# Performance work log

Hardware: AMD Instinct MI355X
Metric: run time of the kernel (lower is better)

## Reference

```python
import jax, jax.numpy as jnp
import numpy as np

N_NODES = 100000


def _gcn_conv(x, edge_index, W, b, n_nodes):
    """PyG GCNConv: add self-loops, symmetric deg^-1/2 normalization,
    linear transform, scatter-sum aggregation, bias."""
    loop = jnp.arange(n_nodes, dtype=edge_index.dtype)
    src = jnp.concatenate([edge_index[0], loop])  # message sources
    dst = jnp.concatenate([edge_index[1], loop])  # message targets
    deg = jax.ops.segment_sum(jnp.ones_like(dst, dtype=x.dtype), dst,
                              num_segments=n_nodes)
    dinv = jnp.where(deg > 0, jax.lax.rsqrt(jnp.maximum(deg, 1.0)), 0.0)
    norm = dinv[src] * dinv[dst]  # [E+N]
    h = x @ W  # [N, out] transform before aggregation (fewer bytes moved)
    msg = h[src] * norm[:, None]  # [E+N, out]
    out = jax.ops.segment_sum(msg, dst, num_segments=n_nodes)
    return out + b


def setup_inputs() -> dict:
    key = jax.random.key(0)
    k1, k2, k3, k4, k5, k6 = jax.random.split(key, 6)
    in_ch, hid, out_ch = 128, 64, 64
    x = jax.random.normal(k1, (N_NODES, in_ch), dtype=jnp.float32)
    edge_index = jax.random.randint(k2, (2, 3200000), 0, N_NODES, dtype=jnp.int64)
    # Glorot-style init for GCN weights, zeros for bias (PyG default)
    W1 = jax.random.normal(k3, (in_ch, hid), dtype=jnp.float32) / np.sqrt(in_ch)
    b1 = jnp.zeros((hid,), dtype=jnp.float32)
    W2 = jax.random.normal(k4, (hid, out_ch), dtype=jnp.float32) / np.sqrt(hid)
    b2 = jnp.zeros((out_ch,), dtype=jnp.float32)
    return {"x": x, "edge_index": edge_index, "W1": W1, "b1": b1,
            "W2": W2, "b2": b2}


def reference(x, edge_index, W1, b1, W2, b2):
    n = x.shape[0]
    h = _gcn_conv(x, edge_index, W1, b1, n)
    h = jax.nn.relu(h)
    out = _gcn_conv(h, edge_index, W2, b2, n)
    return out
```

## Files before the change

### kernel.cpp

```cpp
#include <hip/hip_runtime.h>
#include <math.h>


#define BKT_SHIFT 9
#define BKT_NODES 512
#define NBSH      256
#define CHUNK     8192
#define MAXB      20480

typedef unsigned short ushort_t;

static __device__ __forceinline__ unsigned short f2bf(float f) {
    unsigned u = __float_as_uint(f);
    unsigned r = (u + 0x7FFFu + ((u >> 16) & 1u)) >> 16;
    return (unsigned short)r;
}
static __device__ __forceinline__ float bf_lo(unsigned u) {
    return __uint_as_float(u << 16);
}
static __device__ __forceinline__ float bf_hi(unsigned u) {
    return __uint_as_float(u & 0xFFFF0000u);
}

struct ushort4_t { unsigned short x, y, z, w; };

__global__ __launch_bounds__(256) void zero_small(int* __restrict__ bhist,
                                                  int* __restrict__ bcur) {
    int t = threadIdx.x;
    bhist[t] = 0;
    bcur[t]  = 0;
}

__global__ __launch_bounds__(256) void coarse_hist(const int* __restrict__ dst,
                                                   int* __restrict__ bhist,
                                                   int E, int NB) {
    __shared__ int h[NBSH];
    const int t  = threadIdx.x;
    const int e0 = blockIdx.x * CHUNK;
    const int n  = min(CHUNK, E - e0);
    h[t] = 0;
    __syncthreads();
    for (int i = t; i < n; i += 256) atomicAdd(&h[dst[e0 + i] >> BKT_SHIFT], 1);
    __syncthreads();
    if (t < NB && h[t] > 0) atomicAdd(&bhist[t], h[t]);
}

__global__ __launch_bounds__(256) void scan196(const int* __restrict__ bhist,
                                               int* __restrict__ boffs, int NB, int E) {
    __shared__ int sh[256];
    int t = threadIdx.x;
    int orig = (t < NB) ? bhist[t] : 0;
    sh[t] = orig;
    __syncthreads();
    for (int d = 1; d < 256; d <<= 1) {
        int u = (t >= d) ? sh[t - d] : 0;
        __syncthreads();
        sh[t] += u;
        __syncthreads();
    }
    if (t < NB) boffs[t] = sh[t] - orig;
    if (t == NB) boffs[NB] = E;
    if (t == 255 && NB < 255) boffs[NB] = E;
}

__global__ __launch_bounds__(256) void bucket_bin(const int* __restrict__ src,
                                                  const int* __restrict__ dst,
                                                  const int* __restrict__ boffs,
                                                  int* __restrict__ bcur,
                                                  unsigned* __restrict__ pairs,
                                                  int E, int NB) {
    __shared__ unsigned stag[CHUNK];
    __shared__ int hist[NBSH];
    __shared__ int lofs[NBSH];
    __shared__ int lcur[NBSH];
    __shared__ int gbase[NBSH];
    const int t  = threadIdx.x;
    const int e0 = blockIdx.x * CHUNK;
    const int n  = min(CHUNK, E - e0);

    for (int i = t; i < NBSH; i += 256) hist[i] = 0;
    __syncthreads();
    for (int i = t; i < n; i += 256) atomicAdd(&hist[dst[e0 + i] >> BKT_SHIFT], 1);
    __syncthreads();
    int v = hist[t];
    lofs[t] = v;
    __syncthreads();
    for (int d = 1; d < 256; d <<= 1) {
        int u = (t >= d) ? lofs[t - d] : 0;
        __syncthreads();
        lofs[t] += u;
        __syncthreads();
    }
    if (t < NB) {
        lcur[t]  = lofs[t] - v;
        gbase[t] = (v > 0) ? boffs[t] + atomicAdd(&bcur[t], v) : 0;
    }
    __syncthreads();
    for (int i = t; i < n; i += 256) {
        int d = dst[e0 + i];
        int s = src[e0 + i];
        int b = d >> BKT_SHIFT;
        int p = atomicAdd(&lcur[b], 1);
        stag[p] = ((unsigned)(d & (BKT_NODES - 1)) << 17) | (unsigned)s;
    }
    __syncthreads();
    const int wv = t >> 6, ln = t & 63;
    for (int b = wv; b < NB; b += 4) {
        int cb = hist[b];
        if (cb == 0) continue;
        int lo = lofs[b] - cb;
        int gb = gbase[b];
        for (int i = ln; i < cb; i += 64) pairs[gb + i] = stag[lo + i];
    }
}

__global__ __launch_bounds__(1024) void csr_sort(const unsigned* __restrict__ pairs,
                                                 const int* __restrict__ boffs,
                                                 int* __restrict__ csr,
                                                 int* __restrict__ cnt,
                                                 int* __restrict__ offs,
                                                 float* __restrict__ dinv,
                                                 int N) {
    extern __shared__ unsigned stag2[];
    __shared__ int lhist[BKT_NODES];
    __shared__ int lofs[BKT_NODES];
    __shared__ int ncur[BKT_NODES];
    const int b    = blockIdx.x;
    const int t    = threadIdx.x;
    const int n0   = b << BKT_SHIFT;
    const int base = boffs[b];
    const int ne   = boffs[b + 1] - base;

    if (t < BKT_NODES) lhist[t] = 0;
    __syncthreads();
    for (int i = t; i < ne; i += 1024) atomicAdd(&lhist[pairs[base + i] >> 17], 1);
    __syncthreads();
    if (t < BKT_NODES) lofs[t] = lhist[t];
    __syncthreads();
    for (int d = 1; d < BKT_NODES; d <<= 1) {
        int u = (t < BKT_NODES && t >= d) ? lofs[t - d] : 0;
        __syncthreads();
        if (t < BKT_NODES) lofs[t] += u;
        __syncthreads();
    }
    if (t < BKT_NODES) {
        int node = n0 + t;
        int ex   = lofs[t] - lhist[t];
        ncur[t]  = ex;
        if (node < N) {
            cnt[node]  = lhist[t];
            offs[node] = base + ex;
            dinv[node] = rsqrtf((float)(lhist[t] + 1));
        }
    }
    __syncthreads();
    if (ne <= MAXB) {
        for (int i = t; i < ne; i += 1024) {
            unsigned p = pairs[base + i];
            int pos = atomicAdd(&ncur[p >> 17], 1);
            stag2[pos] = p & 0x1FFFFu;
        }
        __syncthreads();
        for (int i = t; i < ne; i += 1024) csr[base + i] = (int)stag2[i];
    } else {
        for (int i = t; i < ne; i += 1024) {
            unsigned p = pairs[base + i];
            int pos = atomicAdd(&ncur[p >> 17], 1);
            csr[base + pos] = (int)(p & 0x1FFFFu);
        }
    }
}

template <int K>
__global__ __launch_bounds__(256) void gemm_scale(const float* __restrict__ X,
                                                  const float* __restrict__ W,
                                                  const float* __restrict__ dinv,
                                                  ushort_t* __restrict__ G, int N) {
    __shared__ float Ws[K * 64];
    __shared__ float Xs[32][K + 1];
    const int t  = threadIdx.x;
    const int r0 = blockIdx.x * 32;

    for (int i = t; i < K * 16; i += 256)
        ((float4*)Ws)[i] = ((const float4*)W)[i];

    for (int i = t; i < 32 * (K / 4); i += 256) {
        int row = i / (K / 4);
        int kk  = (i % (K / 4)) * 4;
        int gr  = r0 + row;
        float4 v = make_float4(0.f, 0.f, 0.f, 0.f);
        if (gr < N) v = *(const float4*)(X + (size_t)gr * K + kk);
        Xs[row][kk + 0] = v.x; Xs[row][kk + 1] = v.y;
        Xs[row][kk + 2] = v.z; Xs[row][kk + 3] = v.w;
    }
    __syncthreads();

    const int cg = (t & 15) * 4;
    const int ry = t >> 4;
    float4 a0 = make_float4(0.f, 0.f, 0.f, 0.f);
    float4 a1 = make_float4(0.f, 0.f, 0.f, 0.f);
#pragma unroll 8
    for (int k = 0; k < K; ++k) {
        float4 w = *(const float4*)&Ws[k * 64 + cg];
        float x0 = Xs[ry][k];
        float x1 = Xs[ry + 16][k];
        a0.x = fmaf(x0, w.x, a0.x); a0.y = fmaf(x0, w.y, a0.y);
        a0.z = fmaf(x0, w.z, a0.z); a0.w = fmaf(x0, w.w, a0.w);
        a1.x = fmaf(x1, w.x, a1.x); a1.y = fmaf(x1, w.y, a1.y);
        a1.z = fmaf(x1, w.z, a1.z); a1.w = fmaf(x1, w.w, a1.w);
    }

    int row0 = r0 + ry;
    if (row0 < N) {
        float s = dinv[row0];
        ushort4_t o = { f2bf(a0.x * s), f2bf(a0.y * s), f2bf(a0.z * s), f2bf(a0.w * s) };
        *(ushort4_t*)(G + (size_t)row0 * 64 + cg) = o;
    }
    int row1 = r0 + ry + 16;
    if (row1 < N) {
        float s = dinv[row1];
        ushort4_t o = { f2bf(a1.x * s), f2bf(a1.y * s), f2bf(a1.z * s), f2bf(a1.w * s) };
        *(ushort4_t*)(G + (size_t)row1 * 64 + cg) = o;
    }
}

__global__ __launch_bounds__(256) void aggregate(const ushort_t* __restrict__ G,
                                                 const int* __restrict__ offs,
                                                 const int* __restrict__ cnt,
                                                 const int* __restrict__ csr,
                                                 const float* __restrict__ dinv,
                                                 const float* __restrict__ bias,
                                                 float* __restrict__ out, int N,
                                                 int do_relu) {
    int w    = (blockIdx.x * 256 + threadIdx.x) >> 6;
    int lane = threadIdx.x & 63;
    if (w >= N) return;
    const int grp = lane >> 3;
    const int sub = lane & 7;
    const int beg = offs[w];
    const int num = cnt[w];

    float acc[8] = {0.f, 0.f, 0.f, 0.f, 0.f, 0.f, 0.f, 0.f};
    if (grp == 0) {
        uint4 v = *(const uint4*)(G + (size_t)w * 64 + sub * 8);
        acc[0] += bf_lo(v.x); acc[1] += bf_hi(v.x);
        acc[2] += bf_lo(v.y); acc[3] += bf_hi(v.y);
        acc[4] += bf_lo(v.z); acc[5] += bf_hi(v.z);
        acc[6] += bf_lo(v.w); acc[7] += bf_hi(v.w);
    }

    int e = 0;
    for (; e + 16 <= num; e += 16) {
        int s0 = csr[beg + e + grp];
        int s1 = csr[beg + e + 8 + grp];
        uint4 v0 = *(const uint4*)(G + (size_t)s0 * 64 + sub * 8);
        uint4 v1 = *(const uint4*)(G + (size_t)s1 * 64 + sub * 8);
        acc[0] += bf_lo(v0.x); acc[1] += bf_hi(v0.x);
        acc[2] += bf_lo(v0.y); acc[3] += bf_hi(v0.y);
        acc[4] += bf_lo(v0.z); acc[5] += bf_hi(v0.z);
        acc[6] += bf_lo(v0.w); acc[7] += bf_hi(v0.w);
        acc[0] += bf_lo(v1.x); acc[1] += bf_hi(v1.x);
        acc[2] += bf_lo(v1.y); acc[3] += bf_hi(v1.y);
        acc[4] += bf_lo(v1.z); acc[5] += bf_hi(v1.z);
        acc[6] += bf_lo(v1.w); acc[7] += bf_hi(v1.w);
    }
    if (e + 8 <= num) {
        int s0 = csr[beg + e + grp];
        uint4 v0 = *(const uint4*)(G + (size_t)s0 * 64 + sub * 8);
        acc[0] += bf_lo(v0.x); acc[1] += bf_hi(v0.x);
        acc[2] += bf_lo(v0.y); acc[3] += bf_hi(v0.y);
        acc[4] += bf_lo(v0.z); acc[5] += bf_hi(v0.z);
        acc[6] += bf_lo(v0.w); acc[7] += bf_hi(v0.w);
        e += 8;
    }
    int rem = num - e;
    if (grp < rem) {
        int s0 = csr[beg + e + grp];
        uint4 v0 = *(const uint4*)(G + (size_t)s0 * 64 + sub * 8);
        acc[0] += bf_lo(v0.x); acc[1] += bf_hi(v0.x);
        acc[2] += bf_lo(v0.y); acc[3] += bf_hi(v0.y);
        acc[4] += bf_lo(v0.z); acc[5] += bf_hi(v0.z);
        acc[6] += bf_lo(v0.w); acc[7] += bf_hi(v0.w);
    }

#pragma unroll
    for (int m = 8; m <= 32; m <<= 1) {
#pragma unroll
        for (int j = 0; j < 8; ++j) acc[j] += __shfl_xor(acc[j], m, 64);
    }

    if (grp == 0) {
        float d = dinv[w];
        float4 bl0 = *(const float4*)(bias + sub * 8);
        float4 bl1 = *(const float4*)(bias + sub * 8 + 4);
        float4 o0 = make_float4(fmaf(acc[0], d, bl0.x), fmaf(acc[1], d, bl0.y),
                                fmaf(acc[2], d, bl0.z), fmaf(acc[3], d, bl0.w));
        float4 o1 = make_float4(fmaf(acc[4], d, bl1.x), fmaf(acc[5], d, bl1.y),
                                fmaf(acc[6], d, bl1.z), fmaf(acc[7], d, bl1.w));
        if (do_relu) {
            o0.x = fmaxf(o0.x, 0.f); o0.y = fmaxf(o0.y, 0.f);
            o0.z = fmaxf(o0.z, 0.f); o0.w = fmaxf(o0.w, 0.f);
            o1.x = fmaxf(o1.x, 0.f); o1.y = fmaxf(o1.y, 0.f);
            o1.z = fmaxf(o1.z, 0.f); o1.w = fmaxf(o1.w, 0.f);
        }
        *(float4*)(out + (size_t)w * 64 + sub * 8)     = o0;
        *(float4*)(out + (size_t)w * 64 + sub * 8 + 4) = o1;
    }
}

extern "C" void kernel_launch(void* const* d_in, const int* in_sizes, int n_in,
                              void* d_out, int out_size, void* d_ws, size_t ws_size,
                              hipStream_t stream) {
    const float* x  = (const float*)d_in[0];
    const int*   ei = (const int*)d_in[1];
    const float* W1 = (const float*)d_in[2];
    const float* b1 = (const float*)d_in[3];
    const float* W2 = (const float*)d_in[4];
    const float* b2 = (const float*)d_in[5];
    float* out = (float*)d_out;

    const int IN_CH = 128;
    const int N = in_sizes[0] / IN_CH;
    const int E = in_sizes[1] / 2;
    const int* src = ei;
    const int* dst = ei + E;
    const int NB = (N + BKT_NODES - 1) >> BKT_SHIFT;

    char* ws = (char*)d_ws;
    size_t off = 0;
    auto take = [&](size_t bytes) -> char* {
        char* p = ws + off;
        off += (bytes + 255) & ~(size_t)255;
        return p;
    };
    int*      cnt   = (int*)take((size_t)N * 4);
    int*      offs  = (int*)take((size_t)N * 4);
    float*    dinv  = (float*)take((size_t)N * 4);
    int*      bhist = (int*)take(NBSH * 4);
    int*      boffs = (int*)take((NBSH + 1) * 4);
    int*      bcur  = (int*)take(NBSH * 4);
    int*      csr   = (int*)take((size_t)E * 4);
    ushort_t* g     = (ushort_t*)take((size_t)E * 4);
    float*    a1    = (float*)take((size_t)N * 64 * 4);
    unsigned* pairs = (unsigned*)g;

    const int nbC = (E + CHUNK - 1) / CHUNK;

    zero_small<<<1, 256, 0, stream>>>(bhist, bcur);
    coarse_hist<<<nbC, 256, 0, stream>>>(dst, bhist, E, NB);
    scan196<<<1, 256, 0, stream>>>(bhist, boffs, NB, E);
    bucket_bin<<<nbC, 256, 0, stream>>>(src, dst, boffs, bcur, pairs, E, NB);
    csr_sort<<<NB, 1024, MAXB * 4, stream>>>(pairs, boffs, csr, cnt, offs, dinv, N);

    gemm_scale<128><<<(N + 31) / 32, 256, 0, stream>>>(x, W1, dinv, g, N);
    aggregate<<<(N + 3) / 4, 256, 0, stream>>>(g, offs, cnt, csr, dinv, b1, a1, N, 1);
    gemm_scale<64><<<(N + 31) / 32, 256, 0, stream>>>(a1, W2, dinv, g, N);
    aggregate<<<(N + 3) / 4, 256, 0, stream>>>(g, offs, cnt, csr, dinv, b2, out, N, 0);
}
```

Measured before the change: 343.0 us.

## Sort CSR neighbours by source range and unroll aggregation gather loop

The per-bucket CSR sort now keys on destination node plus the high bits of the source index, so each node's neighbour list is roughly sorted by source. This should improve cache locality of the gathers in aggregation. The aggregation loop is unrolled to issue four independent row loads per iteration, and the small zeroing kernel is replaced by a memset plus zeroing bcur inside the scan kernel. The cost is an 8192-bin shared histogram and a 1024-wide scan in the sort kernel, which adds shared memory and synchronisation.

```diff
diff --git a/kernel.cpp b/kernel.cpp
--- a/kernel.cpp
+++ b/kernel.cpp
@@ -7,6 +7,8 @@
 #define NBSH      256
 #define CHUNK     8192
 #define MAXB      20480
+#define RSH       13
+#define NBIN      8192
 
 typedef unsigned short ushort_t;
 
@@ -23,13 +25,6 @@
 }
 
 struct ushort4_t { unsigned short x, y, z, w; };
-
-__global__ __launch_bounds__(256) void zero_small(int* __restrict__ bhist,
-                                                  int* __restrict__ bcur) {
-    int t = threadIdx.x;
-    bhist[t] = 0;
-    bcur[t]  = 0;
-}
 
 __global__ __launch_bounds__(256) void coarse_hist(const int* __restrict__ dst,
                                                    int* __restrict__ bhist,
@@ -46,9 +41,11 @@
 }
 
 __global__ __launch_bounds__(256) void scan196(const int* __restrict__ bhist,
-                                               int* __restrict__ boffs, int NB, int E) {
+                                               int* __restrict__ boffs,
+                                               int* __restrict__ bcur, int NB, int E) {
     __shared__ int sh[256];
     int t = threadIdx.x;
+    bcur[t] = 0;
     int orig = (t < NB) ? bhist[t] : 0;
     sh[t] = orig;
     __syncthreads();
@@ -114,60 +111,82 @@
     }
 }
 
-__global__ __launch_bounds__(1024) void csr_sort(const unsigned* __restrict__ pairs,
-                                                 const int* __restrict__ boffs,
-                                                 int* __restrict__ csr,
-                                                 int* __restrict__ cnt,
-                                                 int* __restrict__ offs,
-                                                 float* __restrict__ dinv,
-                                                 int N) {
-    extern __shared__ unsigned stag2[];
-    __shared__ int lhist[BKT_NODES];
-    __shared__ int lofs[BKT_NODES];
-    __shared__ int ncur[BKT_NODES];
+__global__ __launch_bounds__(1024) void csr_sort2(const unsigned* __restrict__ pairs,
+                                                  const int* __restrict__ boffs,
+                                                  unsigned* __restrict__ csr,
+                                                  int* __restrict__ cnt,
+                                                  int* __restrict__ offs,
+                                                  float* __restrict__ dinv,
+                                                  int N) {
+    extern __shared__ unsigned st[];
+    __shared__ int hist2[NBIN];
+    __shared__ int sc[1024];
     const int b    = blockIdx.x;
     const int t    = threadIdx.x;
     const int n0   = b << BKT_SHIFT;
     const int base = boffs[b];
     const int ne   = boffs[b + 1] - base;
 
-    if (t < BKT_NODES) lhist[t] = 0;
-    __syncthreads();
-    for (int i = t; i < ne; i += 1024) atomicAdd(&lhist[pairs[base + i] >> 17], 1);
-    __syncthreads();
-    if (t < BKT_NODES) lofs[t] = lhist[t];
-    __syncthreads();
-    for (int d = 1; d < BKT_NODES; d <<= 1) {
-        int u = (t < BKT_NODES && t >= d) ? lofs[t - d] : 0;
-        __syncthreads();
-        if (t < BKT_NODES) lofs[t] += u;
-        __syncthreads();
-    }
+    for (int i = t; i < NBIN; i += 1024) hist2[i] = 0;
+    __syncthreads();
+    for (int i = t; i < ne; i += 1024) {
+        unsigned p = pairs[base + i];
+        int key = (int)(((p >> 17) << 4) | ((p & 0x1FFFFu) >> RSH));
+        atomicAdd(&hist2[key], 1);
+    }
+    __syncthreads();
     if (t < BKT_NODES) {
         int node = n0 + t;
-        int ex   = lofs[t] - lhist[t];
-        ncur[t]  = ex;
         if (node < N) {
-            cnt[node]  = lhist[t];
-            offs[node] = base + ex;
-            dinv[node] = rsqrtf((float)(lhist[t] + 1));
+            int d = 0;
+#pragma unroll
+            for (int r = 0; r < 16; ++r) d += hist2[(t << 4) + r];
+            cnt[node]  = d;
+            dinv[node] = rsqrtf((float)(d + 1));
         }
     }
     __syncthreads();
-    if (ne <= MAXB) {
-        for (int i = t; i < ne; i += 1024) {
-            unsigned p = pairs[base + i];
-            int pos = atomicAdd(&ncur[p >> 17], 1);
-            stag2[pos] = p & 0x1FFFFu;
-        }
-        __syncthreads();
-        for (int i = t; i < ne; i += 1024) csr[base + i] = (int)stag2[i];
-    } else {
-        for (int i = t; i < ne; i += 1024) {
-            unsigned p = pairs[base + i];
-            int pos = atomicAdd(&ncur[p >> 17], 1);
-            csr[base + pos] = (int)(p & 0x1FFFFu);
-        }
+    int lv[8];
+    int lsum = 0;
+#pragma unroll
+    for (int j = 0; j < 8; ++j) {
+        int v = hist2[(t << 3) + j];
+        lv[j] = v;
+        lsum += v;
+    }
+    sc[t] = lsum;
+    __syncthreads();
+    for (int d = 1; d < 1024; d <<= 1) {
+        int u = (t >= d) ? sc[t - d] : 0;
+        __syncthreads();
+        sc[t] += u;
+        __syncthreads();
+    }
+    int run = sc[t] - lsum;
+    __syncthreads();
+#pragma unroll
+    for (int j = 0; j < 8; ++j) {
+        hist2[(t << 3) + j] = run;
+        run += lv[j];
+    }
+    __syncthreads();
+    if (t < BKT_NODES) {
+        int node = n0 + t;
+        if (node < N) offs[node] = base + hist2[t << 4];
+    }
+    __syncthreads();
+    const bool fit = (ne <= MAXB);
+    for (int i = t; i < ne; i += 1024) {
+        unsigned p = pairs[base + i];
+        int key = (int)(((p >> 17) << 4) | ((p & 0x1FFFFu) >> RSH));
+        int pos = atomicAdd(&hist2[key], 1);
+        unsigned sv = p & 0x1FFFFu;
+        if (fit) st[pos] = sv;
+        else     csr[base + pos] = sv;
+    }
+    if (fit) {
+        __syncthreads();
+        for (int i = t; i < ne; i += 1024) csr[base + i] = st[i];
     }
 }
 
@@ -224,14 +243,20 @@
     }
 }
 
-__global__ __launch_bounds__(256) void aggregate(const ushort_t* __restrict__ G,
-                                                 const int* __restrict__ offs,
-                                                 const int* __restrict__ cnt,
-                                                 const int* __restrict__ csr,
-                                                 const float* __restrict__ dinv,
-                                                 const float* __restrict__ bias,
-                                                 float* __restrict__ out, int N,
-                                                 int do_relu) {
+#define ACC8(v)                                         \
+    acc[0] += bf_lo((v).x); acc[1] += bf_hi((v).x);     \
+    acc[2] += bf_lo((v).y); acc[3] += bf_hi((v).y);     \
+    acc[4] += bf_lo((v).z); acc[5] += bf_hi((v).z);     \
+    acc[6] += bf_lo((v).w); acc[7] += bf_hi((v).w);
+
+__global__ __launch_bounds__(256) void aggregate5(const ushort_t* __restrict__ G,
+                                                  const int* __restrict__ offs,
+                                                  const int* __restrict__ cnt,
+                                                  const unsigned* __restrict__ csr,
+                                                  const float* __restrict__ dinv,
+                                                  const float* __restrict__ bias,
+                                                  float* __restrict__ out, int N,
+                                                  int do_relu) {
     int w    = (blockIdx.x * 256 + threadIdx.x) >> 6;
     int lane = threadIdx.x & 63;
     if (w >= N) return;
@@ -243,44 +268,40 @@
     float acc[8] = {0.f, 0.f, 0.f, 0.f, 0.f, 0.f, 0.f, 0.f};
     if (grp == 0) {
         uint4 v = *(const uint4*)(G + (size_t)w * 64 + sub * 8);
-        acc[0] += bf_lo(v.x); acc[1] += bf_hi(v.x);
-        acc[2] += bf_lo(v.y); acc[3] += bf_hi(v.y);
-        acc[4] += bf_lo(v.z); acc[5] += bf_hi(v.z);
-        acc[6] += bf_lo(v.w); acc[7] += bf_hi(v.w);
+        ACC8(v);
     }
 
     int e = 0;
-    for (; e + 16 <= num; e += 16) {
-        int s0 = csr[beg + e + grp];
-        int s1 = csr[beg + e + 8 + grp];
-        uint4 v0 = *(const uint4*)(G + (size_t)s0 * 64 + sub * 8);
-        uint4 v1 = *(const uint4*)(G + (size_t)s1 * 64 + sub * 8);
-        acc[0] += bf_lo(v0.x); acc[1] += bf_hi(v0.x);
-        acc[2] += bf_lo(v0.y); acc[3] += bf_hi(v0.y);
-        acc[4] += bf_lo(v0.z); acc[5] += bf_hi(v0.z);
-        acc[6] += bf_lo(v0.w); acc[7] += bf_hi(v0.w);
-        acc[0] += bf_lo(v1.x); acc[1] += bf_hi(v1.x);
-        acc[2] += bf_lo(v1.y); acc[3] += bf_hi(v1.y);
-        acc[4] += bf_lo(v1.z); acc[5] += bf_hi(v1.z);
-        acc[6] += bf_lo(v1.w); acc[7] += bf_hi(v1.w);
+    for (; e + 32 <= num; e += 32) {
+        unsigned s0 = csr[beg + e + grp];
+        unsigned s1 = csr[beg + e + 8 + grp];
+        unsigned s2 = csr[beg + e + 16 + grp];
+        unsigned s3 = csr[beg + e + 24 + grp];
+        uint4 v0 = *(const uint4*)(G + ((size_t)s0 << 6) + (sub << 3));
+        uint4 v1 = *(const uint4*)(G + ((size_t)s1 << 6) + (sub << 3));
+        uint4 v2 = *(const uint4*)(G + ((size_t)s2 << 6) + (sub << 3));
+        uint4 v3 = *(const uint4*)(G + ((size_t)s3 << 6) + (sub << 3));
+        ACC8(v0); ACC8(v1); ACC8(v2); ACC8(v3);
+    }
+    if (e + 16 <= num) {
+        unsigned s0 = csr[beg + e + grp];
+        unsigned s1 = csr[beg + e + 8 + grp];
+        uint4 v0 = *(const uint4*)(G + ((size_t)s0 << 6) + (sub << 3));
+        uint4 v1 = *(const uint4*)(G + ((size_t)s1 << 6) + (sub << 3));
+        ACC8(v0); ACC8(v1);
+        e += 16;
     }
     if (e + 8 <= num) {
-        int s0 = csr[beg + e + grp];
-        uint4 v0 = *(const uint4*)(G + (size_t)s0 * 64 + sub * 8);
-        acc[0] += bf_lo(v0.x); acc[1] += bf_hi(v0.x);
-        acc[2] += bf_lo(v0.y); acc[3] += bf_hi(v0.y);
-        acc[4] += bf_lo(v0.z); acc[5] += bf_hi(v0.z);
-        acc[6] += bf_lo(v0.w); acc[7] += bf_hi(v0.w);
+        unsigned s0 = csr[beg + e + grp];
+        uint4 v0 = *(const uint4*)(G + ((size_t)s0 << 6) + (sub << 3));
+        ACC8(v0);
         e += 8;
     }
     int rem = num - e;
     if (grp < rem) {
-        int s0 = csr[beg + e + grp];
-        uint4 v0 = *(const uint4*)(G + (size_t)s0 * 64 + sub * 8);
-        acc[0] += bf_lo(v0.x); acc[1] += bf_hi(v0.x);
-        acc[2] += bf_lo(v0.y); acc[3] += bf_hi(v0.y);
-        acc[4] += bf_lo(v0.z); acc[5] += bf_hi(v0.z);
-        acc[6] += bf_lo(v0.w); acc[7] += bf_hi(v0.w);
+        unsigned s0 = csr[beg + e + grp];
+        uint4 v0 = *(const uint4*)(G + ((size_t)s0 << 6) + (sub << 3));
+        ACC8(v0);
     }
 
 #pragma unroll
@@ -333,27 +354,27 @@
         off += (bytes + 255) & ~(size_t)255;
         return p;
     };
+    float*    dinv  = (float*)take((size_t)N * 4);
     int*      cnt   = (int*)take((size_t)N * 4);
     int*      offs  = (int*)take((size_t)N * 4);
-    float*    dinv  = (float*)take((size_t)N * 4);
     int*      bhist = (int*)take(NBSH * 4);
     int*      boffs = (int*)take((NBSH + 1) * 4);
     int*      bcur  = (int*)take(NBSH * 4);
-    int*      csr   = (int*)take((size_t)E * 4);
+    unsigned* csr   = (unsigned*)take((size_t)E * 4);
     ushort_t* g     = (ushort_t*)take((size_t)E * 4);
     float*    a1    = (float*)take((size_t)N * 64 * 4);
     unsigned* pairs = (unsigned*)g;
 
     const int nbC = (E + CHUNK - 1) / CHUNK;
 
-    zero_small<<<1, 256, 0, stream>>>(bhist, bcur);
+    hipMemsetAsync(bhist, 0, NBSH * 4, stream);
     coarse_hist<<<nbC, 256, 0, stream>>>(dst, bhist, E, NB);
-    scan196<<<1, 256, 0, stream>>>(bhist, boffs, NB, E);
+    scan196<<<1, 256, 0, stream>>>(bhist, boffs, bcur, NB, E);
     bucket_bin<<<nbC, 256, 0, stream>>>(src, dst, boffs, bcur, pairs, E, NB);
-    csr_sort<<<NB, 1024, MAXB * 4, stream>>>(pairs, boffs, csr, cnt, offs, dinv, N);
+    csr_sort2<<<NB, 1024, MAXB * 4, stream>>>(pairs, boffs, csr, cnt, offs, dinv, N);
 
     gemm_scale<128><<<(N + 31) / 32, 256, 0, stream>>>(x, W1, dinv, g, N);
-    aggregate<<<(N + 3) / 4, 256, 0, stream>>>(g, offs, cnt, csr, dinv, b1, a1, N, 1);
+    aggregate5<<<(N + 3) / 4, 256, 0, stream>>>(g, offs, cnt, csr, dinv, b1, a1, N, 1);
     gemm_scale<64><<<(N + 31) / 32, 256, 0, stream>>>(a1, W2, dinv, g, N);
-    aggregate<<<(N + 3) / 4, 256, 0, stream>>>(g, offs, cnt, csr, dinv, b2, out, N, 0);
-}
+    aggregate5<<<(N + 3) / 4, 256, 0, stream>>>(g, offs, cnt, csr, dinv, b2, out, N, 0);
+}
```

After: 337.5 us. No clear change (-1.6%).
